# Optimization experiments

Hardware: AMD Instinct MI355X
Metric: run time of the kernel (lower is better)

## Reference

```python
import jax, jax.numpy as jnp
import numpy as np
from jax import lax

R = 1          # box-filter radius
EPS = 1e-06    # regularizer


def boxfilter(z, r=R):
    """ReplicationPad2d(r) + depthwise (groups=C) mean conv with kernel (2r+1)^2."""
    k = 2 * r + 1
    c = z.shape[1]
    zp = jnp.pad(z, ((0, 0), (0, 0), (r, r), (r, r)), mode='edge')  # replication pad
    w = jnp.full((c, 1, k, k), 1.0 / (k * k), dtype=z.dtype)        # [O, I/g, kh, kw]
    return lax.conv_general_dilated(zp, w, window_strides=(1, 1), padding='VALID',
                                    feature_group_count=c)


def setup_inputs() -> dict:
    key = jax.random.key(0)
    kx, ky = jax.random.split(key)
    shape = (8, 3, 1024, 1024)
    # image-valued inputs in [0, 255), matching the final clamp range
    x = jax.random.uniform(kx, shape, jnp.float32, 0.0, 255.0)
    y = jax.random.uniform(ky, shape, jnp.float32, 0.0, 255.0)
    return {"x": x, "y": y}


def reference(x, y):
    mean_x = boxfilter(x)
    mean_y = boxfilter(y)
    cov_xy = boxfilter(x * y) - mean_x * mean_y
    var_x = boxfilter(x * x) - mean_x * mean_x
    A = cov_xy / (var_x + EPS)
    b = mean_y - A * mean_x
    res = boxfilter(A) * x + boxfilter(b)
    # torch: res.int() truncates toward zero, clamp(0,255), back to float
    return jnp.clip(jnp.trunc(res), 0.0, 255.0)
```

## Files before the change

kernel.cpp:

```cpp
#include <hip/hip_runtime.h>


#define NSTRIP 5
#define SOUT 252
#define TH 44
#define NIT (TH + 4)

__device__ __forceinline__ float dpp_prev(float v) {
  return __int_as_float(__builtin_amdgcn_update_dpp(
      0, __float_as_int(v), 0x138, 0xF, 0xF, false));
}
__device__ __forceinline__ float dpp_next(float v) {
  return __int_as_float(__builtin_amdgcn_update_dpp(
      0, __float_as_int(v), 0x130, 0xF, 0xF, false));
}

__global__ __launch_bounds__(256) void gf_kernel(const float* __restrict__ xg,
                                                 const float* __restrict__ yg,
                                                 float* __restrict__ outg,
                                                 const int H, const int W,
                                                 const int nchunk) {
  const int tid = threadIdx.x;
  const int l = tid & 63;
  const int gw = (blockIdx.x << 2) + (tid >> 6);
  const int per_img = NSTRIP * nchunk;
  const int img = gw / per_img;
  const int rem = gw - img * per_img;
  const int chunk = rem / NSTRIP;
  const int strip = rem - chunk * NSTRIP;
  const int c0 = strip * SOUT;
  const int oy0 = min(chunk * TH, H - TH);
  const size_t base = (size_t)img * H * W;

  const int oc0 = c0 - 2 + 4 * l;
  const int cc0 = min(max(oc0, 0), W - 1);
  const int cc1 = min(max(oc0 + 1, 0), W - 1);
  const int cc2 = min(max(oc0 + 2, 0), W - 1);
  const int cc3 = min(max(oc0 + 3, 0), W - 1);
  const bool p0 = (l >= 1) && (oc0 < W);
  const bool p1 = (l <= 62) && (oc0 + 2 < W);
  const bool eL2 = (oc0 + 2 == 0);
  const bool eR1 = (oc0 + 1 == W - 1);
  const bool tfixw = (oy0 == 0);
  const bool bfixw = (oy0 + TH == H);

  const float inv9 = 1.0f / 9.0f;

  float hx[3][4], hy[3][4], hxy[3][4], hxx[3][4];
  float sa[3][4], sb[3][4], xr3[3][4];
  float nx[4], ny[4];

  {
    const int rn_ = min(max(oy0 - 2, 0), H - 1);
    const float* xr_ = xg + base + (size_t)rn_ * W;
    const float* yr_ = yg + base + (size_t)rn_ * W;
    nx[0] = xr_[cc0]; nx[1] = xr_[cc1]; nx[2] = xr_[cc2]; nx[3] = xr_[cc3];
    ny[0] = yr_[cc0]; ny[1] = yr_[cc1]; ny[2] = yr_[cc2]; ny[3] = yr_[cc3];
  }

#define BODY(S, PS, NS, I, DO_A, DO_OUT, DO_TFIX, DO_BFIX)                     \
  {                                                                            \
    const int i_ = (I);                                                        \
    const int rr_ = oy0 - 2 + i_;                                              \
    float cx[4], cy[4];                                                        \
    _Pragma("unroll") for (int j = 0; j < 4; ++j) {                            \
      cx[j] = nx[j];                                                           \
      cy[j] = ny[j];                                                           \
    }                                                                          \
    {      \
      const int rn_ = min(max(rr_ + 1, 0), H - 1);                             \
      const float* xr_ = xg + base + (size_t)rn_ * W;                          \
      const float* yr_ = yg + base + (size_t)rn_ * W;                          \
      nx[0] = xr_[cc0]; nx[1] = xr_[cc1]; nx[2] = xr_[cc2]; nx[3] = xr_[cc3];  \
      ny[0] = yr_[cc0]; ny[1] = yr_[cc1]; ny[2] = yr_[cc2]; ny[3] = yr_[cc3];  \
    }                                                                          \
    const float xm_ = dpp_prev(cx[3]), xp_ = dpp_next(cx[0]);                  \
    const float ym_ = dpp_prev(cy[3]), yp_ = dpp_next(cy[0]);                  \
    hx[S][0] = xm_ + cx[0] + cx[1];                                            \
    hy[S][0] = ym_ + cy[0] + cy[1];                                            \
    hxy[S][0] = xm_ * ym_ + cx[0] * cy[0] + cx[1] * cy[1];                     \
    hxx[S][0] = xm_ * xm_ + cx[0] * cx[0] + cx[1] * cx[1];                     \
    hx[S][1] = cx[0] + cx[1] + cx[2];                                          \
    hy[S][1] = cy[0] + cy[1] + cy[2];                                          \
    hxy[S][1] = cx[0] * cy[0] + cx[1] * cy[1] + cx[2] * cy[2];                 \
    hxx[S][1] = cx[0] * cx[0] + cx[1] * cx[1] + cx[2] * cx[2];                 \
    hx[S][2] = cx[1] + cx[2] + cx[3];                                          \
    hy[S][2] = cy[1] + cy[2] + cy[3];                                          \
    hxy[S][2] = cx[1] * cy[1] + cx[2] * cy[2] + cx[3] * cy[3];                 \
    hxx[S][2] = cx[1] * cx[1] + cx[2] * cx[2] + cx[3] * cx[3];                 \
    hx[S][3] = cx[2] + cx[3] + xp_;                                            \
    hy[S][3] = cy[2] + cy[3] + yp_;                                            \
    hxy[S][3] = cx[2] * cy[2] + cx[3] * cy[3] + xp_ * yp_;                     \
    hxx[S][3] = cx[2] * cx[2] + cx[3] * cx[3] + xp_ * xp_;                     \
    _Pragma("unroll") for (int j = 0; j < 4; ++j) xr3[S][j] = cx[j];           \
    if (DO_A) {                                          \
      float A_[4], B_[4];                                                      \
      _Pragma("unroll") for (int j = 0; j < 4; ++j) {                          \
        const float Sx = hx[0][j] + hx[1][j] + hx[2][j];                       \
        const float Sy = hy[0][j] + hy[1][j] + hy[2][j];                       \
        const float Sxy = hxy[0][j] + hxy[1][j] + hxy[2][j];                   \
        const float Sxx = hxx[0][j] + hxx[1][j] + hxx[2][j];                   \
        const float mx = Sx * inv9, my = Sy * inv9;                            \
        const float cov = Sxy * inv9 - mx * my;                                \
        const float var = Sxx * inv9 - mx * mx;                                \
        const float d_ = var + 1e-6f;                                          \
        float v_ = __builtin_amdgcn_rcpf(d_);                                  \
        v_ = v_ + v_ * (1.0f - d_ * v_);                                       \
        A_[j] = cov * v_;                                                      \
        B_[j] = my - A_[j] * mx;                                               \
      }                                                                        \
      const float Am_ = dpp_prev(A_[3]), Ap_ = dpp_next(A_[0]);                \
      const float Bm_ = dpp_prev(B_[3]), Bp_ = dpp_next(B_[0]);                \
      sa[S][0] = Am_ + A_[0] + A_[1];                                          \
      sb[S][0] = Bm_ + B_[0] + B_[1];                                          \
      sa[S][1] = A_[0] + A_[1] + (eR1 ? A_[1] : A_[2]);                        \
      sb[S][1] = B_[0] + B_[1] + (eR1 ? B_[1] : B_[2]);                        \
      sa[S][2] = (eL2 ? A_[2] : A_[1]) + A_[2] + A_[3];                        \
      sb[S][2] = (eL2 ? B_[2] : B_[1]) + B_[2] + B_[3];                        \
      sa[S][3] = A_[2] + A_[3] + Ap_;                                          \
      sb[S][3] = B_[2] + B_[3] + Bp_;                                          \
      if (DO_TFIX && tfixw) {                               \
        _Pragma("unroll") for (int j = 0; j < 4; ++j) {                        \
          sa[PS][j] = sa[S][j];                                                \
          sb[PS][j] = sb[S][j];                                                \
        }                                                                      \
      }                                                                        \
      if (DO_BFIX && bfixw) {                              \
        _Pragma("unroll") for (int j = 0; j < 4; ++j) {                        \
          sa[S][j] = sa[PS][j];                                                \
          sb[S][j] = sb[PS][j];                                                \
        }                                                                      \
      }                                                                        \
      if (DO_OUT) {                                      \
        float* orow_ = outg + base + (size_t)(rr_ - 2) * W;                    \
        float o_[4];                                                           \
        _Pragma("unroll") for (int j = 0; j < 4; ++j) {                        \
          const float SA = sa[0][j] + sa[1][j] + sa[2][j];                     \
          const float SB = sb[0][j] + sb[1][j] + sb[2][j];                     \
          const float res = (SA * xr3[NS][j] + SB) * inv9;                     \
          o_[j] = fminf(fmaxf(truncf(res), 0.0f), 255.0f);                     \
        }                                                                      \
        if (p0) {                                                              \
          float2 v2; v2.x = o_[0]; v2.y = o_[1];                               \
          *(float2*)(orow_ + oc0) = v2;                                        \
        }                                                                      \
        if (p1) {                                                              \
          float2 v2; v2.x = o_[2]; v2.y = o_[3];                               \
          *(float2*)(orow_ + (oc0 + 2)) = v2;                                  \
        }                                                                      \
      }                                                                        \
    }                                                                          \
  }

  BODY(0, 2, 1, 0, 0, 0, 0, 0)
  BODY(1, 0, 2, 1, 0, 0, 0, 0)
  BODY(2, 1, 0, 2, 1, 0, 0, 0)
  BODY(0, 2, 1, 3, 1, 0, 1, 0)
  BODY(1, 0, 2, 4, 1, 1, 0, 0)
  BODY(2, 1, 0, 5, 1, 1, 0, 0)
  for (int ii = 6; ii <= NIT - 6; ii += 3) {
    BODY(0, 2, 1, ii, 1, 1, 0, 0)
    BODY(1, 0, 2, ii + 1, 1, 1, 0, 0)
    BODY(2, 1, 0, ii + 2, 1, 1, 0, 0)
  }
  BODY(0, 2, 1, NIT - 3, 1, 1, 0, 0)
  BODY(1, 0, 2, NIT - 2, 1, 1, 0, 0)
  BODY(2, 1, 0, NIT - 1, 1, 1, 0, 1)
#undef BODY
}

extern "C" void kernel_launch(void* const* d_in, const int* in_sizes, int n_in,
                              void* d_out, int out_size, void* d_ws, size_t ws_size,
                              hipStream_t stream) {
  const float* x = (const float*)d_in[0];
  const float* y = (const float*)d_in[1];
  float* out = (float*)d_out;
  const int H = 1024, W = 1024;
  const int imgs = in_sizes[0] / (H * W);
  const int nchunk = (H + TH - 1) / TH;
  const int waves = imgs * NSTRIP * nchunk;
  dim3 block(256, 1, 1);
  dim3 grid(waves / 4, 1, 1);
  gf_kernel<<<grid, block, 0, stream>>>(x, y, out, H, W, nchunk);
}
```

Baseline: 284.9 us.

## Align lane columns to 16B for float4 loads/stores and shrink row tile

Shifts each lane's four-column group so it starts on a 4-aligned column. Scalar clamped loads become single float4 loads per row, and the split float2 stores become one float4 store. Out-of-range lanes fill their registers with the replicated edge value, and the edge handling in the second box filter moves to new left/right flags. The row tile shrinks from 44 to 20 and the strip width from 252 to 248. This raises the vertical halo overhead (4 extra rows per 20 output rows) but gives more waves.

```diff
diff --git a/kernel.cpp b/kernel.cpp
--- a/kernel.cpp
+++ b/kernel.cpp
@@ -2,8 +2,8 @@
 
 
 #define NSTRIP 5
-#define SOUT 252
-#define TH 44
+#define SOUT 248
+#define TH 20
 #define NIT (TH + 4)
 
 __device__ __forceinline__ float dpp_prev(float v) {
@@ -32,15 +32,12 @@
   const int oy0 = min(chunk * TH, H - TH);
   const size_t base = (size_t)img * H * W;
 
-  const int oc0 = c0 - 2 + 4 * l;
-  const int cc0 = min(max(oc0, 0), W - 1);
-  const int cc1 = min(max(oc0 + 1, 0), W - 1);
-  const int cc2 = min(max(oc0 + 2, 0), W - 1);
-  const int cc3 = min(max(oc0 + 3, 0), W - 1);
-  const bool p0 = (l >= 1) && (oc0 < W);
-  const bool p1 = (l <= 62) && (oc0 + 2 < W);
-  const bool eL2 = (oc0 + 2 == 0);
-  const bool eR1 = (oc0 + 1 == W - 1);
+  const int k0 = c0 - 4 + 4 * l;
+  const bool inr = (k0 >= 0) && (k0 <= W - 4);
+  const int cedge = (k0 < 0) ? 0 : (W - 1);
+  const bool own = (l >= 1) && (l <= 62) && (k0 + 3 <= W - 1);
+  const bool eL0 = (k0 == 0);
+  const bool eR3 = (k0 == W - 4);
   const bool tfixw = (oy0 == 0);
   const bool bfixw = (oy0 + TH == H);
 
@@ -50,13 +47,24 @@
   float sa[3][4], sb[3][4], xr3[3][4];
   float nx[4], ny[4];
 
-  {
-    const int rn_ = min(max(oy0 - 2, 0), H - 1);
-    const float* xr_ = xg + base + (size_t)rn_ * W;
-    const float* yr_ = yg + base + (size_t)rn_ * W;
-    nx[0] = xr_[cc0]; nx[1] = xr_[cc1]; nx[2] = xr_[cc2]; nx[3] = xr_[cc3];
-    ny[0] = yr_[cc0]; ny[1] = yr_[cc1]; ny[2] = yr_[cc2]; ny[3] = yr_[cc3];
+#define LDROW(RIDX)                                                          \
+  {                                                                          \
+    const int rn_ = min(max((RIDX), 0), H - 1);                              \
+    const float* xr_ = xg + base + (size_t)rn_ * W;                          \
+    const float* yr_ = yg + base + (size_t)rn_ * W;                          \
+    if (inr) {                                                               \
+      const float4 vx_ = *(const float4*)(xr_ + k0);                         \
+      const float4 vy_ = *(const float4*)(yr_ + k0);                         \
+      nx[0] = vx_.x; nx[1] = vx_.y; nx[2] = vx_.z; nx[3] = vx_.w;            \
+      ny[0] = vy_.x; ny[1] = vy_.y; ny[2] = vy_.z; ny[3] = vy_.w;            \
+    } else {                                                                 \
+      const float sx_ = xr_[cedge], sy_ = yr_[cedge];                        \
+      nx[0] = nx[1] = nx[2] = nx[3] = sx_;                                   \
+      ny[0] = ny[1] = ny[2] = ny[3] = sy_;                                   \
+    }                                                                        \
   }
+
+  LDROW(oy0 - 2)
 
 #define BODY(S, PS, NS, I, DO_A, DO_OUT, DO_TFIX, DO_BFIX)                     \
   {                                                                            \
@@ -67,13 +75,7 @@
       cx[j] = nx[j];                                                           \
       cy[j] = ny[j];                                                           \
     }                                                                          \
-    {      \
-      const int rn_ = min(max(rr_ + 1, 0), H - 1);                             \
-      const float* xr_ = xg + base + (size_t)rn_ * W;                          \
-      const float* yr_ = yg + base + (size_t)rn_ * W;                          \
-      nx[0] = xr_[cc0]; nx[1] = xr_[cc1]; nx[2] = xr_[cc2]; nx[3] = xr_[cc3];  \
-      ny[0] = yr_[cc0]; ny[1] = yr_[cc1]; ny[2] = yr_[cc2]; ny[3] = yr_[cc3];  \
-    }                                                                          \
+    LDROW(rr_ + 1)    \
     const float xm_ = dpp_prev(cx[3]), xp_ = dpp_next(cx[0]);                  \
     const float ym_ = dpp_prev(cy[3]), yp_ = dpp_next(cy[0]);                  \
     hx[S][0] = xm_ + cx[0] + cx[1];                                            \
@@ -111,14 +113,14 @@
       }                                                                        \
       const float Am_ = dpp_prev(A_[3]), Ap_ = dpp_next(A_[0]);                \
       const float Bm_ = dpp_prev(B_[3]), Bp_ = dpp_next(B_[0]);                \
-      sa[S][0] = Am_ + A_[0] + A_[1];                                          \
-      sb[S][0] = Bm_ + B_[0] + B_[1];                                          \
-      sa[S][1] = A_[0] + A_[1] + (eR1 ? A_[1] : A_[2]);                        \
-      sb[S][1] = B_[0] + B_[1] + (eR1 ? B_[1] : B_[2]);                        \
-      sa[S][2] = (eL2 ? A_[2] : A_[1]) + A_[2] + A_[3];                        \
-      sb[S][2] = (eL2 ? B_[2] : B_[1]) + B_[2] + B_[3];                        \
-      sa[S][3] = A_[2] + A_[3] + Ap_;                                          \
-      sb[S][3] = B_[2] + B_[3] + Bp_;                                          \
+      sa[S][0] = (eL0 ? A_[0] : Am_) + A_[0] + A_[1];                          \
+      sb[S][0] = (eL0 ? B_[0] : Bm_) + B_[0] + B_[1];                          \
+      sa[S][1] = A_[0] + A_[1] + A_[2];                                        \
+      sb[S][1] = B_[0] + B_[1] + B_[2];                                        \
+      sa[S][2] = A_[1] + A_[2] + A_[3];                                        \
+      sb[S][2] = B_[1] + B_[2] + B_[3];                                        \
+      sa[S][3] = A_[2] + A_[3] + (eR3 ? A_[3] : Ap_);                          \
+      sb[S][3] = B_[2] + B_[3] + (eR3 ? B_[3] : Bp_);                          \
       if (DO_TFIX && tfixw) {                               \
         _Pragma("unroll") for (int j = 0; j < 4; ++j) {                        \
           sa[PS][j] = sa[S][j];                                                \
@@ -132,7 +134,6 @@
         }                                                                      \
       }                                                                        \
       if (DO_OUT) {                                      \
-        float* orow_ = outg + base + (size_t)(rr_ - 2) * W;                    \
         float o_[4];                                                           \
         _Pragma("unroll") for (int j = 0; j < 4; ++j) {                        \
           const float SA = sa[0][j] + sa[1][j] + sa[2][j];                     \
@@ -140,13 +141,10 @@
           const float res = (SA * xr3[NS][j] + SB) * inv9;                     \
           o_[j] = fminf(fmaxf(truncf(res), 0.0f), 255.0f);                     \
         }                                                                      \
-        if (p0) {                                                              \
-          float2 v2; v2.x = o_[0]; v2.y = o_[1];                               \
-          *(float2*)(orow_ + oc0) = v2;                                        \
-        }                                                                      \
-        if (p1) {                                                              \
-          float2 v2; v2.x = o_[2]; v2.y = o_[3];                               \
-          *(float2*)(orow_ + (oc0 + 2)) = v2;                                  \
+        if (own) {                                                             \
+          float4 o4_;                                                          \
+          o4_.x = o_[0]; o4_.y = o_[1]; o4_.z = o_[2]; o4_.w = o_[3];          \
+          *(float4*)(outg + base + (size_t)(rr_ - 2) * W + k0) = o4_;          \
         }                                                                      \
       }                                                                        \
     }                                                                          \
@@ -167,6 +165,7 @@
   BODY(1, 0, 2, NIT - 2, 1, 1, 0, 0)
   BODY(2, 1, 0, NIT - 1, 1, 1, 0, 1)
 #undef BODY
+#undef LDROW
 }
 
 extern "C" void kernel_launch(void* const* d_in, const int* in_sizes, int n_in,
```

New measurement: 333.1 us. +16.9%, slower.
